# Kernel tuning notes

Hardware: AMD Instinct MI355X
Metric: run time of the kernel (lower is better)

## Reference

```python
import jax, jax.numpy as jnp
import numpy as np

N, C, T, V = 32, 128, 128, 25
HS, HT, CI = 3, 2, 32
BN_INV = float(1.0 / np.sqrt(1.0 + 1e-5))  # eval-mode BN: running_mean=0, running_var=1


def conv1x1(x, w, b):
    # x: (N,C,T,V), w: (O,C), b: (O,)
    return jnp.einsum('nctv,oc->notv', x, w) + b[None, :, None, None]


def bn(x, g, b):
    return x * (g * BN_INV)[None, :, None, None] + b[None, :, None, None]


def lrelu(x):
    return jax.nn.leaky_relu(x, 0.1)


def setup_inputs() -> dict:
    key = jax.random.key(0)
    ks = jax.random.split(key, 16)
    w = lambda k, shp: jax.random.normal(k, shp, dtype=jnp.float32) * 0.05
    inp = {
        'x': jax.random.normal(ks[0], (N, C, T, V), dtype=jnp.float32),
        # spatial attention QK projection (conv 1x1): 2*HS*CI out channels
        'w_in_s': w(ks[1], (2 * HS * CI, C)), 'b_in_s': jnp.zeros((2 * HS * CI,), jnp.float32),
        'attention0s': jnp.ones((1, HS, V, V), jnp.float32) / V,
        'alphas': jnp.ones((1, HS, 1, 1), jnp.float32),
        'w_out_s': w(ks[2], (C, HS * C)), 'b_out_s': jnp.zeros((C,), jnp.float32),
        'g_out_s': jnp.ones((C,), jnp.float32), 'be_out_s': jnp.zeros((C,), jnp.float32),
        'w_ff_s': w(ks[3], (C, C)), 'b_ff_s': jnp.zeros((C,), jnp.float32),
        'g_ff_s': jnp.ones((C,), jnp.float32), 'be_ff_s': jnp.zeros((C,), jnp.float32),
        # temporal attention QK projection: 4*HT*CI out channels
        'w_in_t': w(ks[4], (4 * HT * CI, C)), 'b_in_t': jnp.zeros((4 * HT * CI,), jnp.float32),
        'alphat_f': jnp.ones((1, HT, 1, 1), jnp.float32),
        'alphat_b': jnp.ones((1, HT, 1, 1), jnp.float32),
        'w_out_t': w(ks[5], (C, 2 * HT * C)), 'b_out_t': jnp.zeros((C,), jnp.float32),
        'g_out_t': jnp.ones((C,), jnp.float32), 'be_out_t': jnp.zeros((C,), jnp.float32),
        'w_ff_t': w(ks[6], (C, C)), 'b_ff_t': jnp.zeros((C,), jnp.float32),
        'g_ff_t': jnp.ones((C,), jnp.float32), 'be_ff_t': jnp.zeros((C,), jnp.float32),
        # TCN: 7x1 temporal conv
        'w_tcn': w(ks[7], (C, C, 7, 1)), 'b_tcn': jnp.zeros((C,), jnp.float32),
        'g_tcn': jnp.ones((C,), jnp.float32), 'be_tcn': jnp.zeros((C,), jnp.float32),
    }
    return inp


def reference(x, w_in_s, b_in_s, attention0s, alphas, w_out_s, b_out_s, g_out_s, be_out_s,
              w_ff_s, b_ff_s, g_ff_s, be_ff_s, w_in_t, b_in_t, alphat_f, alphat_b,
              w_out_t, b_out_t, g_out_t, be_out_t, w_ff_t, b_ff_t, g_ff_t, be_ff_t,
              w_tcn, b_tcn, g_tcn, be_tcn):
    n = x.shape[0]
    # ---------------- spatial attention (S_atten='free', glo_reg_s) ----------------
    att_bias = attention0s[:, :, None]            # (1,HS,1,V,V) broadcast over T
    alphas_u = alphas[:, :, None]                 # (1,HS,1,1,1)
    qk = conv1x1(x, w_in_s, b_in_s).reshape(n, 2 * HS, CI, T, V)
    q, k = qk[:, :HS], qk[:, HS:]
    att = att_bias + jnp.tanh(jnp.einsum('nsctu,nsctv->nstuv', q, k) / CI) * alphas_u  # (N,HS,T,V,V)
    y = jnp.einsum('nctu,nstuv->nsctv', x, att).reshape(n, HS * C, T, V)
    y = bn(conv1x1(y, w_out_s, b_out_s), g_out_s, be_out_s)
    y = lrelu(x + y)                               # downs1 = identity (in==out, stride 1)
    y = bn(conv1x1(y, w_ff_s, b_ff_s), g_ff_s, be_ff_s)
    s_out = lrelu(x + y)                           # downs2 = identity
    # ---------------- temporal attention (directed, T_atten='context') ----------------
    z_in = s_out                                   # parallel=False -> temporal eats s_out
    qk_t = conv1x1(z_in, w_in_t, b_in_t).reshape(n, 4 * HT, CI, T, V)
    qt, kt = qk_t[:, :2 * HT], qk_t[:, 2 * HT:]
    qt = qt.mean(-1)                               # context attention: mean over joints -> (N,2HT,CI,T)
    kt = kt.mean(-1)
    att_t = jnp.tanh(jnp.einsum('nsct,nscu->nstu', qt, kt) / CI)  # (N,2HT,T,T)
    backward_mask = jnp.triu(jnp.ones((T, T), jnp.float32))
    forward_mask = backward_mask.T
    att_f = att_t[:, :HT] * alphat_f * forward_mask
    att_b = att_t[:, HT:] * alphat_b * backward_mask
    att_t = jnp.concatenate([att_f, att_b], axis=1)               # (N,2HT,T,T)
    z = jnp.einsum('nctv,nstu->nscuv', z_in, att_t).reshape(n, 2 * HT * C, T, V)
    z = bn(conv1x1(z, w_out_t, b_out_t), g_out_t, be_out_t)
    z = lrelu(z_in + z)                            # downt1 = identity
    z = bn(conv1x1(z, w_ff_t, b_ff_t), g_ff_t, be_ff_t)
    t_out = lrelu(z_in + z)                        # downt2 = identity
    # ---------------- TCN branch ----------------
    z2 = jax.lax.conv_general_dilated(t_out, w_tcn, (1, 1), ((3, 3), (0, 0)),
                                      dimension_numbers=('NCHW', 'OIHW', 'NCHW'))
    z2 = bn(z2 + b_tcn[None, :, None, None] * 0 + b_tcn[None, :, None, None], g_tcn, be_tcn) if False else bn(z2 + b_tcn[None, :, None, None], g_tcn, be_tcn)
    out = lrelu(t_out + z2)                        # downtTCN = identity
    return out
```

## Files before the change

### kernel.cpp

```cpp
#include <hip/hip_runtime.h>
#include <cstddef>

#define Nn 32
#define Cc 128
#define Tt 128
#define Vv 25
#define BN_INV 0.9999950000374997f


typedef __attribute__((ext_vector_type(8))) short bf16x8;
typedef __attribute__((ext_vector_type(4))) float f32x4;

__device__ __forceinline__ unsigned short f2bf(float f) {
    union { float f; unsigned u; } x; x.f = f;
    return (unsigned short)((x.u + 0x7FFFu + ((x.u >> 16) & 1u)) >> 16);
}
__device__ __forceinline__ float bf2f(unsigned short s) {
    union { unsigned u; float f; } x; x.u = ((unsigned)s) << 16;
    return x.f;
}

template<int BMODE, int DMODE, int OM>
__global__ __launch_bounds__(256, 2) void gemm_k(
    const unsigned short* __restrict__ A, const void* __restrict__ Bv,
    float* __restrict__ D, unsigned short* __restrict__ Dbf,
    const float* __restrict__ resp, const float* __restrict__ bias,
    const float* __restrict__ gg, const float* __restrict__ bb,
    int M, int K, int lda, int ldb, int ldd,
    long an_stride, long bn_stride, long dn_stride, int gn)
{
    __shared__ short Al[8*64*8];
    __shared__ short Bl[8*64*8];

    const int n  = blockIdx.y;
    const int mt = blockIdx.x / gn;
    const int nt = blockIdx.x - mt*gn;
    const int m0 = mt*128;
    const int j0 = nt*128;

    const unsigned short* An = A + (size_t)n*an_stride;

    const int tid = threadIdx.x;
    const int wav = tid >> 6, lane = tid & 63;
    const int lq = lane >> 4, l16 = lane & 15;

    const int sm  = tid >> 1, skh = tid & 1;
    const int scol = tid & 127, skq = tid >> 7;
    const int bcol = j0 + scol;

    int bo = 0, bv_ = 0;
    if (BMODE == 3) { bo = bcol/25; bv_ = bcol - 25*bo; }

    f32x4 acc[2][8];
    #pragma unroll
    for (int i = 0; i < 2; ++i)
        #pragma unroll
        for (int c = 0; c < 8; ++c) acc[i][c] = (f32x4){0.f,0.f,0.f,0.f};

    for (int k0 = 0; k0 < K; k0 += 32) {
        bf16x8 a0 = (bf16x8){0,0,0,0,0,0,0,0}, a1 = a0;
        {
            int mg = m0 + sm;
            if (mg < M) {
                const unsigned short* ap = An + (size_t)mg*lda + k0 + skh*16;
                a0 = *(const bf16x8*)ap;
                a1 = *(const bf16x8*)(ap + 8);
            }
        }
        unsigned short bq[16];
        if (BMODE == 0) {
            const unsigned short* Bn = (const unsigned short*)Bv + (size_t)n*bn_stride;
            #pragma unroll
            for (int j = 0; j < 16; ++j)
                bq[j] = Bn[(size_t)(k0 + skq*16 + j)*ldb + bcol];
        } else if (BMODE == 4) {
            const float* Bf = (const float*)Bv + (size_t)n*bn_stride;
            #pragma unroll
            for (int j = 0; j < 16; ++j)
                bq[j] = f2bf(Bf[(size_t)(k0 + skq*16 + j)*ldb + bcol]);
        } else if (BMODE == 1) {
            const unsigned short* Bn = (const unsigned short*)Bv + (size_t)n*bn_stride;
            int kb = k0 + skq*16;
            int kidx = kb >> 7, c0 = kb & 127;
            int e = bcol + (kidx - 3)*25;
            bool ok = ((unsigned)e < 3200u);
            #pragma unroll
            for (int j = 0; j < 16; ++j)
                bq[j] = ok ? Bn[(size_t)(c0 + j)*3200 + e] : (unsigned short)0;
        } else {
            const unsigned short* Bn = (const unsigned short*)Bv + (size_t)n*bn_stride;
            int kb = k0 + skq*16;
            int h = kb >> 7, t0 = kb & 127;
            const unsigned short* bp = Bn + (size_t)h*409600 + (size_t)bo*3200
                                          + (size_t)t0*25 + bv_;
            #pragma unroll
            for (int j = 0; j < 16; ++j) bq[j] = bp[j*25];
        }

        __syncthreads();
        {
            short* Ap = Al + ((size_t)((sm>>4)*64 + (sm&15) + 32*skh))*8;
            *(bf16x8*)Ap = a0;
            *(bf16x8*)(Ap + 128) = a1;
        }
        {
            short* Bp = Bl + ((size_t)((scol>>4)*64 + (scol&15) + 32*skq))*8;
            bf16x8 p0, p1;
            #pragma unroll
            for (int j = 0; j < 8; ++j) { p0[j] = (short)bq[j]; p1[j] = (short)bq[8+j]; }
            *(bf16x8*)Bp = p0;
            *(bf16x8*)(Bp + 128) = p1;
        }
        __syncthreads();

        bf16x8 afr[2], bfr[8];
        afr[0] = *(const bf16x8*)(Al + ((size_t)((2*wav+0)*64 + lane))*8);
        afr[1] = *(const bf16x8*)(Al + ((size_t)((2*wav+1)*64 + lane))*8);
        #pragma unroll
        for (int c = 0; c < 8; ++c)
            bfr[c] = *(const bf16x8*)(Bl + ((size_t)(c*64 + lane))*8);
        #pragma unroll
        for (int i = 0; i < 2; ++i)
            #pragma unroll
            for (int c = 0; c < 8; ++c)
                acc[i][c] = __builtin_amdgcn_mfma_f32_16x16x32_bf16(
                    afr[i], bfr[c], acc[i][c], 0, 0, 0);
    }

    #pragma unroll
    for (int i = 0; i < 2; ++i) {
        const int mbase = m0 + (2*wav + i)*16 + lq*4;
        #pragma unroll
        for (int ct = 0; ct < 8; ++ct) {
            const int col = j0 + ct*16 + l16;
            if (DMODE == 0) {
                #pragma unroll
                for (int r = 0; r < 4; ++r) {
                    const int mg = mbase + r;
                    if (mg < M) {
                        const size_t addr = (size_t)mg*ldd + col + (size_t)n*dn_stride;
                        float val = acc[i][ct][r] + (bias ? bias[mg] : 0.f);
                        if (gg) {
                            val = val*(gg[mg]*BN_INV) + bb[mg] + resp[addr];
                            val = val > 0.f ? val : 0.1f*val;
                        }
                        if (OM != 1) D[addr] = val;
                        if (OM >= 1) Dbf[addr] = f2bf(val);
                    }
                }
            } else {
                const int c = col/25, v = col - 25*c;
                const float bi = bias ? bias[c] : 0.f;
                float gv = 0.f, b2 = 0.f;
                if (gg) { gv = gg[c]*BN_INV; b2 = bb[c]; }
                #pragma unroll
                for (int r = 0; r < 4; ++r) {
                    const int u = mbase + r;
                    const size_t addr = (size_t)c*3200 + (size_t)u*25 + v
                                      + (size_t)n*dn_stride;
                    float val = acc[i][ct][r] + bi;
                    if (gg) {
                        val = val*gv + b2 + resp[addr];
                        val = val > 0.f ? val : 0.1f*val;
                    }
                    if (OM != 1) D[addr] = val;
                    if (OM >= 1) Dbf[addr] = f2bf(val);
                }
            }
        }
    }
}

__global__ void k_prep(const float* __restrict__ wis, const float* __restrict__ wos,
                       const float* __restrict__ wfs, const float* __restrict__ wit,
                       const float* __restrict__ wot, const float* __restrict__ wft,
                       const float* __restrict__ wtc, unsigned short* __restrict__ W) {
    int i = blockIdx.x*256 + threadIdx.x;
    if (i < 24576) { W[i] = f2bf(wis[i]); return; }          i -= 24576;
    if (i < 49152) { W[24576 + i] = f2bf(wos[i]); return; }  i -= 49152;
    if (i < 16384) { W[73728 + i] = f2bf(wfs[i]); return; }  i -= 16384;
    if (i < 32768) { W[90112 + i] = f2bf(wit[i]); return; }  i -= 32768;
    if (i < 65536) {
        int ho = i >> 7, c = i & 127; int h = ho >> 7, o = ho & 127;
        W[122880 + i] = f2bf(wot[o*512 + h*128 + c]); return; } i -= 65536;
    if (i < 16384) { W[188416 + i] = f2bf(wft[i]); return; } i -= 16384;
    if (i < 114688) {
        int o = i / 896; int r = i - o*896; int kidx = r >> 7, c = r & 127;
        W[204800 + i] = f2bf(wtc[(o*128 + c)*7 + kidx]); }
}

__global__ void k_att_s(const unsigned short* __restrict__ qk,
                        const float* __restrict__ att0,
                        const float* __restrict__ alphas,
                        unsigned short* __restrict__ att) {
    int b = blockIdx.x;
    int n = b / (3*Tt); int rem = b - n*(3*Tt); int s = rem / Tt; int t = rem - s*Tt;
    __shared__ float qs[32*Vv], ks[32*Vv];
    const unsigned short* qp = qk + (size_t)n*614400 + (size_t)(s*32)*3200 + t*25;
    const unsigned short* kp = qk + (size_t)n*614400 + (size_t)(96 + s*32)*3200 + t*25;
    for (int i = threadIdx.x; i < 32*Vv; i += 256) {
        int c = i / Vv, v = i - c*Vv;
        qs[i] = bf2f(qp[(size_t)c*3200 + v]);
        ks[i] = bf2f(kp[(size_t)c*3200 + v]);
    }
    __syncthreads();
    float alpha = alphas[s];
    for (int i = threadIdx.x; i < Vv*Vv; i += 256) {
        int u = i / Vv, v = i - u*Vv;
        float a = 0.f;
        #pragma unroll
        for (int c = 0; c < 32; ++c) a += qs[c*Vv + u] * ks[c*Vv + v];
        att[(size_t)n*240000 + (size_t)s*80000 + (size_t)t*625 + i] =
            f2bf(att0[s*625 + i] + tanhf(a * (1.f/32.f)) * alpha);
    }
}

__global__ __launch_bounds__(256, 2) void k_eins_mfma(
    const float* __restrict__ X, const unsigned short* __restrict__ att,
    unsigned short* __restrict__ y2)
{
    __shared__ short Xf[128*128];
    __shared__ short Bf[7*4*64*8];

    const int n  = blockIdx.x >> 5;
    const int t0 = (blockIdx.x & 31) * 4;
    const int tid = threadIdx.x;
    const int wav = tid >> 6, lane = tid & 63;
    const int lq = lane >> 4, l16 = lane & 15;

    for (int i = tid; i < 7*4*64; i += 256)
        *(bf16x8*)(Bf + (size_t)i*8) = (bf16x8){0,0,0,0,0,0,0,0};

    const float* xp = X + (size_t)n*409600;
    for (int i = tid; i < 8192; i += 256) {
        int u2 = (i & 15)*2, tl = (i >> 4) & 3, c = i >> 6;
        float f0 = 0.f, f1 = 0.f;
        if (u2 < 25) {
            const float* p = xp + (size_t)c*3200 + (t0 + tl)*25 + u2;
            f0 = p[0];
            if (u2 < 24) f1 = p[1];
        }
        unsigned pk = (unsigned)f2bf(f0) | ((unsigned)f2bf(f1) << 16);
        int byte = (i*4) ^ ((c & 7) << 4);
        *(unsigned*)((char*)Xf + byte) = pk;
    }
    __syncthreads();

    bf16x8 afr[2][4];
    #pragma unroll
    for (int i = 0; i < 2; ++i) {
        const int c = (2*wav + i)*16 + l16;
        #pragma unroll
        for (int ks = 0; ks < 4; ++ks) {
            int byte = ((c*128 + ks*32 + lq*8)*2) ^ ((c & 7) << 4);
            afr[i][ks] = *(const bf16x8*)((const char*)Xf + byte);
        }
    }

    for (int s = 0; s < 3; ++s) {
        const unsigned short* ap = att + (size_t)n*240000 + (size_t)s*80000
                                       + (size_t)t0*625;
        for (int j = tid; j < 2500; j += 256) {
            int tl = j / 625, r = j - tl*625;
            int u = r / 25, v = r - u*25;
            int col = tl*25 + v;
            int l = ((u >> 3) << 4) | (col & 15);
            int nt = col >> 4;
            Bf[(size_t)((nt*4 + tl)*64 + l)*8 + (u & 7)] = (short)ap[j];
        }
        __syncthreads();

        f32x4 acc[2][7];
        #pragma unroll
        for (int i = 0; i < 2; ++i)
            #pragma unroll
            for (int nt = 0; nt < 7; ++nt) acc[i][nt] = (f32x4){0.f,0.f,0.f,0.f};

        #pragma unroll
        for (int ks = 0; ks < 4; ++ks) {
            bf16x8 bfr[7];
            #pragma unroll
            for (int nt = 0; nt < 7; ++nt)
                bfr[nt] = *(const bf16x8*)(Bf + (size_t)((nt*4 + ks)*64 + lane)*8);
            #pragma unroll
            for (int i = 0; i < 2; ++i)
                #pragma unroll
                for (int nt = 0; nt < 7; ++nt)
                    acc[i][nt] = __builtin_amdgcn_mfma_f32_16x16x32_bf16(
                        afr[i][ks], bfr[nt], acc[i][nt], 0, 0, 0);
        }

        unsigned short* yb = y2 + (size_t)n*1228800 + (size_t)(s*128)*3200 + t0*25;
        #pragma unroll
        for (int i = 0; i < 2; ++i) {
            const int row = (2*wav + i)*16 + lq*4;
            #pragma unroll
            for (int nt = 0; nt < 7; ++nt) {
                const int col = nt*16 + l16;
                if (col < 100) {
                    unsigned short* yp = yb + (size_t)row*3200 + col;
                    #pragma unroll
                    for (int r = 0; r < 4; ++r)
                        yp[(size_t)r*3200] = f2bf(acc[i][nt][r]);
                }
            }
        }
        __syncthreads();
    }
}

__global__ void k_mean(const float* __restrict__ X, unsigned short* __restrict__ xb) {
    int idx = blockIdx.x*256 + threadIdx.x;
    if (idx >= Nn*Cc*Tt) return;
    const float* p = X + (size_t)idx*25;
    float s = 0.f;
    #pragma unroll
    for (int v = 0; v < Vv; ++v) s += p[v];
    xb[idx] = f2bf(s * (1.f/25.f));
}

__global__ void k_att_t(const float* __restrict__ qkt, const float* __restrict__ af,
                        const float* __restrict__ ab, unsigned short* __restrict__ attb) {
    int n = blockIdx.x >> 2, h = blockIdx.x & 3;
    __shared__ float qs[32*Tt], ks[32*Tt];
    const float* qp = qkt + (size_t)n*32768 + (size_t)(h*32)*128;
    const float* kp = qkt + (size_t)n*32768 + (size_t)(128 + h*32)*128;
    for (int i = threadIdx.x; i < 32*Tt; i += 256) { qs[i] = qp[i]; ks[i] = kp[i]; }
    __syncthreads();
    float alpha = (h < 2) ? af[h] : ab[h-2];
    for (int i = threadIdx.x; i < Tt*Tt; i += 256) {
        int u = i >> 7, t = i & 127;
        bool keep = (h < 2) ? (t >= u) : (t <= u);
        float val = 0.f;
        if (keep) {
            float a = 0.f;
            #pragma unroll
            for (int c = 0; c < 32; ++c) a += qs[c*Tt + t] * ks[c*Tt + u];
            val = tanhf(a * (1.f/32.f)) * alpha;
        }
        attb[(size_t)n*65536 + (size_t)u*512 + h*128 + t] = f2bf(val);
    }
}

extern "C" void kernel_launch(void* const* d_in, const int* in_sizes, int n_in,
                              void* d_out, int out_size, void* d_ws, size_t ws_size,
                              hipStream_t stream) {
    const float* x       = (const float*)d_in[0];
    const float* w_in_s  = (const float*)d_in[1];
    const float* b_in_s  = (const float*)d_in[2];
    const float* att0s   = (const float*)d_in[3];
    const float* alphas  = (const float*)d_in[4];
    const float* w_out_s = (const float*)d_in[5];
    const float* b_out_s = (const float*)d_in[6];
    const float* g_out_s = (const float*)d_in[7];
    const float* be_out_s= (const float*)d_in[8];
    const float* w_ff_s  = (const float*)d_in[9];
    const float* b_ff_s  = (const float*)d_in[10];
    const float* g_ff_s  = (const float*)d_in[11];
    const float* be_ff_s = (const float*)d_in[12];
    const float* w_in_t  = (const float*)d_in[13];
    const float* b_in_t  = (const float*)d_in[14];
    const float* alphat_f= (const float*)d_in[15];
    const float* alphat_b= (const float*)d_in[16];
    const float* w_out_t = (const float*)d_in[17];
    const float* b_out_t = (const float*)d_in[18];
    const float* g_out_t = (const float*)d_in[19];
    const float* be_out_t= (const float*)d_in[20];
    const float* w_ff_t  = (const float*)d_in[21];
    const float* b_ff_t  = (const float*)d_in[22];
    const float* g_ff_t  = (const float*)d_in[23];
    const float* be_ff_t = (const float*)d_in[24];
    const float* w_tcn   = (const float*)d_in[25];
    const float* b_tcn   = (const float*)d_in[26];
    const float* g_tcn   = (const float*)d_in[27];
    const float* be_tcn  = (const float*)d_in[28];

    hipMemsetAsync(d_ws, 0, ws_size, stream);

    float* ws = (float*)d_ws;
    unsigned short* WB    = (unsigned short*)ws;
    unsigned short* QKBF  = (unsigned short*)(ws + 200000);
    unsigned short* S1BF  = (unsigned short*)(ws + 200000);
    unsigned short* ATSB  = (unsigned short*)(ws + 10030400);
    unsigned short* Y2BF  = (unsigned short*)(ws + 13870400);
    float*          SOUT  = ws + 33531200;
    unsigned short* ATTB  = (unsigned short*)(ws + 200000);
    unsigned short* XBARB = (unsigned short*)(ws + 1300000);
    float*          QKT   = ws + 1600000;
    unsigned short* TMPB  = (unsigned short*)(ws + 2700000);
    unsigned short* T1BF  = (unsigned short*)(ws + 46638400);
    float*          TOUT  = ws + 2700000;
    unsigned short* TOUTB = (unsigned short*)(ws + 15810000);
    float* out = (float*)d_out;

    unsigned short* wbis = WB;
    unsigned short* wbos = WB + 24576;
    unsigned short* wbfs = WB + 73728;
    unsigned short* wbit = WB + 90112;
    unsigned short* wbot = WB + 122880;
    unsigned short* wbft = WB + 188416;
    unsigned short* wbtc = WB + 204800;

    dim3 blk(256);
    const float* NUL = nullptr;

    k_prep<<<1248, blk, 0, stream>>>(w_in_s, w_out_s, w_ff_s, w_in_t,
                                     w_out_t, w_ff_t, w_tcn, WB);

    gemm_k<4,0,1><<<dim3(50,32), blk, 0, stream>>>(
        wbis, x, nullptr, QKBF, NUL, b_in_s, NUL, NUL,
        192, 128, 128, 3200, 3200, 0L, 409600L, 614400L, 25);
    k_att_s<<<Nn*3*Tt, blk, 0, stream>>>(QKBF, att0s, alphas, ATSB);
    k_eins_mfma<<<dim3(Nn*32), blk, 0, stream>>>(x, ATSB, Y2BF);
    gemm_k<0,0,1><<<dim3(25,32), blk, 0, stream>>>(
        wbos, Y2BF, nullptr, S1BF, x, b_out_s, g_out_s, be_out_s,
        128, 384, 384, 3200, 3200, 0L, 1228800L, 409600L, 25);
    gemm_k<0,0,0><<<dim3(25,32), blk, 0, stream>>>(
        wbfs, S1BF, SOUT, nullptr, x, b_ff_s, g_ff_s, be_ff_s,
        128, 128, 128, 3200, 3200, 0L, 409600L, 409600L, 25);

    k_mean<<<2048, blk, 0, stream>>>(SOUT, XBARB);
    gemm_k<0,0,0><<<dim3(2,32), blk, 0, stream>>>(
        wbit, XBARB, QKT, nullptr, NUL, b_in_t, NUL, NUL,
        256, 128, 128, 128, 128, 0L, 16384L, 32768L, 1);
    k_att_t<<<Nn*4, blk, 0, stream>>>(QKT, alphat_f, alphat_b, ATTB);
    gemm_k<4,0,1><<<dim3(100,32), blk, 0, stream>>>(
        wbot, SOUT, nullptr, TMPB, NUL, NUL, NUL, NUL,
        512, 128, 128, 3200, 3200, 0L, 409600L, 1638400L, 25);
    gemm_k<3,2,1><<<dim3(25,32), blk, 0, stream>>>(
        ATTB, TMPB, nullptr, T1BF, SOUT, b_out_t, g_out_t, be_out_t,
        128, 512, 512, 3200, 3200, 65536L, 1638400L, 409600L, 25);
    gemm_k<0,0,2><<<dim3(25,32), blk, 0, stream>>>(
        wbft, T1BF, TOUT, TOUTB, SOUT, b_ff_t, g_ff_t, be_ff_t,
        128, 128, 128, 3200, 3200, 0L, 409600L, 409600L, 25);

    gemm_k<1,0,0><<<dim3(25,32), blk, 0, stream>>>(
        wbtc, TOUTB, out, nullptr, TOUT, b_tcn, g_tcn, be_tcn,
        128, 896, 896, 3200, 3200, 0L, 409600L, 409600L, 25);
}
```

Measured before the change: 762.7 us.

## Halve GEMM N-tile to 64 and prefetch next K-slice into registers

The shared GEMM kernel now uses a 128x64 output tile instead of 128x128, which doubles the grid size for every GEMM launch and raises launch bounds to four blocks per SM. It also adds register double-buffering: the next K-slice's A and B values are loaded from global memory after the LDS barrier, so those loads overlap the MFMA work on the current slice. The aim is more occupancy and latency hiding for these memory-bound 1x1-conv GEMMs. The cost is lower data reuse per tile (A is re-read twice as often) and more register pressure under the tighter launch bound.

```diff
diff --git a/kernel.cpp b/kernel.cpp
--- a/kernel.cpp
+++ b/kernel.cpp
@@ -20,8 +20,50 @@
     return x.f;
 }
 
+
+#define GFETCH(K0)                                                             \
+    {                                                                          \
+        int mg = m0 + sm;                                                      \
+        if (mg < M) {                                                          \
+            const unsigned short* ap = An + (size_t)mg*lda + (K0) + skh*16;    \
+            a0n = *(const bf16x8*)ap;                                          \
+            a1n = *(const bf16x8*)(ap + 8);                                    \
+        }                                                                      \
+        if (BMODE == 0) {                                                      \
+            const unsigned short* Bn = (const unsigned short*)Bv               \
+                                     + (size_t)n*bn_stride;                    \
+            _Pragma("unroll")                                                  \
+            for (int j = 0; j < 8; ++j)                                        \
+                bqn[j] = Bn[(size_t)((K0) + skq*8 + j)*ldb + bcol];            \
+        } else if (BMODE == 4) {                                               \
+            const float* Bf = (const float*)Bv + (size_t)n*bn_stride;          \
+            _Pragma("unroll")                                                  \
+            for (int j = 0; j < 8; ++j)                                        \
+                bqn[j] = f2bf(Bf[(size_t)((K0) + skq*8 + j)*ldb + bcol]);      \
+        } else if (BMODE == 1) {                                               \
+            const unsigned short* Bn = (const unsigned short*)Bv               \
+                                     + (size_t)n*bn_stride;                    \
+            int kb = (K0) + skq*8;                                             \
+            int kidx = kb >> 7, c0 = kb & 127;                                 \
+            int e = bcol + (kidx - 3)*25;                                      \
+            bool ok = ((unsigned)e < 3200u);                                   \
+            _Pragma("unroll")                                                  \
+            for (int j = 0; j < 8; ++j)                                        \
+                bqn[j] = ok ? Bn[(size_t)(c0 + j)*3200 + e] : (unsigned short)0;\
+        } else {                                                  \
+            const unsigned short* Bn = (const unsigned short*)Bv               \
+                                     + (size_t)n*bn_stride;                    \
+            int kb = (K0) + skq*8;                                             \
+            int h = kb >> 7, t0b = kb & 127;                                   \
+            const unsigned short* bp = Bn + (size_t)h*409600 + (size_t)bo*3200 \
+                                          + (size_t)t0b*25 + bv_;              \
+            _Pragma("unroll")                                                  \
+            for (int j = 0; j < 8; ++j) bqn[j] = bp[j*25];                     \
+        }                                                                      \
+    }
+
 template<int BMODE, int DMODE, int OM>
-__global__ __launch_bounds__(256, 2) void gemm_k(
+__global__ __launch_bounds__(256, 4) void gemm_k(
     const unsigned short* __restrict__ A, const void* __restrict__ Bv,
     float* __restrict__ D, unsigned short* __restrict__ Dbf,
     const float* __restrict__ resp, const float* __restrict__ bias,
@@ -30,13 +72,13 @@
     long an_stride, long bn_stride, long dn_stride, int gn)
 {
     __shared__ short Al[8*64*8];
-    __shared__ short Bl[8*64*8];
+    __shared__ short Bl[4*64*8];
 
     const int n  = blockIdx.y;
     const int mt = blockIdx.x / gn;
     const int nt = blockIdx.x - mt*gn;
     const int m0 = mt*128;
-    const int j0 = nt*128;
+    const int j0 = nt*64;
 
     const unsigned short* An = A + (size_t)n*an_stride;
 
@@ -45,84 +87,50 @@
     const int lq = lane >> 4, l16 = lane & 15;
 
     const int sm  = tid >> 1, skh = tid & 1;
-    const int scol = tid & 127, skq = tid >> 7;
+    const int scol = tid & 63, skq = tid >> 6;
     const int bcol = j0 + scol;
 
     int bo = 0, bv_ = 0;
     if (BMODE == 3) { bo = bcol/25; bv_ = bcol - 25*bo; }
 
-    f32x4 acc[2][8];
+    f32x4 acc[2][4];
     #pragma unroll
     for (int i = 0; i < 2; ++i)
         #pragma unroll
-        for (int c = 0; c < 8; ++c) acc[i][c] = (f32x4){0.f,0.f,0.f,0.f};
+        for (int c = 0; c < 4; ++c) acc[i][c] = (f32x4){0.f,0.f,0.f,0.f};
+
+    bf16x8 a0n = (bf16x8){0,0,0,0,0,0,0,0}, a1n = a0n;
+    unsigned short bqn[8];
+    GFETCH(0);
 
     for (int k0 = 0; k0 < K; k0 += 32) {
-        bf16x8 a0 = (bf16x8){0,0,0,0,0,0,0,0}, a1 = a0;
-        {
-            int mg = m0 + sm;
-            if (mg < M) {
-                const unsigned short* ap = An + (size_t)mg*lda + k0 + skh*16;
-                a0 = *(const bf16x8*)ap;
-                a1 = *(const bf16x8*)(ap + 8);
-            }
-        }
-        unsigned short bq[16];
-        if (BMODE == 0) {
-            const unsigned short* Bn = (const unsigned short*)Bv + (size_t)n*bn_stride;
-            #pragma unroll
-            for (int j = 0; j < 16; ++j)
-                bq[j] = Bn[(size_t)(k0 + skq*16 + j)*ldb + bcol];
-        } else if (BMODE == 4) {
-            const float* Bf = (const float*)Bv + (size_t)n*bn_stride;
-            #pragma unroll
-            for (int j = 0; j < 16; ++j)
-                bq[j] = f2bf(Bf[(size_t)(k0 + skq*16 + j)*ldb + bcol]);
-        } else if (BMODE == 1) {
-            const unsigned short* Bn = (const unsigned short*)Bv + (size_t)n*bn_stride;
-            int kb = k0 + skq*16;
-            int kidx = kb >> 7, c0 = kb & 127;
-            int e = bcol + (kidx - 3)*25;
-            bool ok = ((unsigned)e < 3200u);
-            #pragma unroll
-            for (int j = 0; j < 16; ++j)
-                bq[j] = ok ? Bn[(size_t)(c0 + j)*3200 + e] : (unsigned short)0;
-        } else {
-            const unsigned short* Bn = (const unsigned short*)Bv + (size_t)n*bn_stride;
-            int kb = k0 + skq*16;
-            int h = kb >> 7, t0 = kb & 127;
-            const unsigned short* bp = Bn + (size_t)h*409600 + (size_t)bo*3200
-                                          + (size_t)t0*25 + bv_;
-            #pragma unroll
-            for (int j = 0; j < 16; ++j) bq[j] = bp[j*25];
-        }
-
         __syncthreads();
         {
             short* Ap = Al + ((size_t)((sm>>4)*64 + (sm&15) + 32*skh))*8;
-            *(bf16x8*)Ap = a0;
-            *(bf16x8*)(Ap + 128) = a1;
+            *(bf16x8*)Ap = a0n;
+            *(bf16x8*)(Ap + 128) = a1n;
         }
         {
-            short* Bp = Bl + ((size_t)((scol>>4)*64 + (scol&15) + 32*skq))*8;
-            bf16x8 p0, p1;
-            #pragma unroll
-            for (int j = 0; j < 8; ++j) { p0[j] = (short)bq[j]; p1[j] = (short)bq[8+j]; }
+            short* Bp = Bl + ((size_t)((scol>>4)*64 + skq*16 + (scol&15)))*8;
+            bf16x8 p0;
+            #pragma unroll
+            for (int j = 0; j < 8; ++j) p0[j] = (short)bqn[j];
             *(bf16x8*)Bp = p0;
-            *(bf16x8*)(Bp + 128) = p1;
         }
         __syncthreads();
 
-        bf16x8 afr[2], bfr[8];
+        if (k0 + 32 < K) GFETCH(k0 + 32);
+
+        bf16x8 afr[2], bfr[4];
         afr[0] = *(const bf16x8*)(Al + ((size_t)((2*wav+0)*64 + lane))*8);
         afr[1] = *(const bf16x8*)(Al + ((size_t)((2*wav+1)*64 + lane))*8);
         #pragma unroll
-        for (int c = 0; c < 8; ++c)
+        for (int c = 0; c < 4; ++c)
             bfr[c] = *(const bf16x8*)(Bl + ((size_t)(c*64 + lane))*8);
         #pragma unroll
         for (int i = 0; i < 2; ++i)
             #pragma unroll
-            for (int c = 0; c < 8; ++c)
+            for (int c = 0; c < 4; ++c)
                 acc[i][c] = __builtin_amdgcn_mfma_f32_16x16x32_bf16(
                     afr[i], bfr[c], acc[i][c], 0, 0, 0);
     }
@@ -131,7 +139,7 @@
     for (int i = 0; i < 2; ++i) {
         const int mbase = m0 + (2*wav + i)*16 + lq*4;
         #pragma unroll
-        for (int ct = 0; ct < 8; ++ct) {
+        for (int ct = 0; ct < 4; ++ct) {
             const int col = j0 + ct*16 + l16;
             if (DMODE == 0) {
                 #pragma unroll
@@ -407,34 +415,34 @@
     k_prep<<<1248, blk, 0, stream>>>(w_in_s, w_out_s, w_ff_s, w_in_t,
                                      w_out_t, w_ff_t, w_tcn, WB);
 
-    gemm_k<4,0,1><<<dim3(50,32), blk, 0, stream>>>(
+    gemm_k<4,0,1><<<dim3(100,32), blk, 0, stream>>>(
         wbis, x, nullptr, QKBF, NUL, b_in_s, NUL, NUL,
-        192, 128, 128, 3200, 3200, 0L, 409600L, 614400L, 25);
+        192, 128, 128, 3200, 3200, 0L, 409600L, 614400L, 50);
     k_att_s<<<Nn*3*Tt, blk, 0, stream>>>(QKBF, att0s, alphas, ATSB);
     k_eins_mfma<<<dim3(Nn*32), blk, 0, stream>>>(x, ATSB, Y2BF);
-    gemm_k<0,0,1><<<dim3(25,32), blk, 0, stream>>>(
+    gemm_k<0,0,1><<<dim3(50,32), blk, 0, stream>>>(
         wbos, Y2BF, nullptr, S1BF, x, b_out_s, g_out_s, be_out_s,
-        128, 384, 384, 3200, 3200, 0L, 1228800L, 409600L, 25);
-    gemm_k<0,0,0><<<dim3(25,32), blk, 0, stream>>>(
+        128, 384, 384, 3200, 3200, 0L, 1228800L, 409600L, 50);
+    gemm_k<0,0,0><<<dim3(50,32), blk, 0, stream>>>(
         wbfs, S1BF, SOUT, nullptr, x, b_ff_s, g_ff_s, be_ff_s,
-        128, 128, 128, 3200, 3200, 0L, 409600L, 409600L, 25);
+        128, 128, 128, 3200, 3200, 0L, 409600L, 409600L, 50);
 
     k_mean<<<2048, blk, 0, stream>>>(SOUT, XBARB);
-    gemm_k<0,0,0><<<dim3(2,32), blk, 0, stream>>>(
+    gemm_k<0,0,0><<<dim3(4,32), blk, 0, stream>>>(
         wbit, XBARB, QKT, nullptr, NUL, b_in_t, NUL, NUL,
-        256, 128, 128, 128, 128, 0L, 16384L, 32768L, 1);
+        256, 128, 128, 128, 128, 0L, 16384L, 32768L, 2);
     k_att_t<<<Nn*4, blk, 0, stream>>>(QKT, alphat_f, alphat_b, ATTB);
-    gemm_k<4,0,1><<<dim3(100,32), blk, 0, stream>>>(
+    gemm_k<4,0,1><<<dim3(200,32), blk, 0, stream>>>(
         wbot, SOUT, nullptr, TMPB, NUL, NUL, NUL, NUL,
-        512, 128, 128, 3200, 3200, 0L, 409600L, 1638400L, 25);
-    gemm_k<3,2,1><<<dim3(25,32), blk, 0, stream>>>(
+        512, 128, 128, 3200, 3200, 0L, 409600L, 1638400L, 50);
+    gemm_k<3,2,1><<<dim3(50,32), blk, 0, stream>>>(
         ATTB, TMPB, nullptr, T1BF, SOUT, b_out_t, g_out_t, be_out_t,
-        128, 512, 512, 3200, 3200, 65536L, 1638400L, 409600L, 25);
-    gemm_k<0,0,2><<<dim3(25,32), blk, 0, stream>>>(
+        128, 512, 512, 3200, 3200, 65536L, 1638400L, 409600L, 50);
+    gemm_k<0,0,2><<<dim3(50,32), blk, 0, stream>>>(
         wbft, T1BF, TOUT, TOUTB, SOUT, b_ff_t, g_ff_t, be_ff_t,
-        128, 128, 128, 3200, 3200, 0L, 409600L, 409600L, 25);
-
-    gemm_k<1,0,0><<<dim3(25,32), blk, 0, stream>>>(
+        128, 128, 128, 3200, 3200, 0L, 409600L, 409600L, 50);
+
+    gemm_k<1,0,0><<<dim3(50,32), blk, 0, stream>>>(
         wbtc, TOUTB, out, nullptr, TOUT, b_tcn, g_tcn, be_tcn,
-        128, 896, 896, 3200, 3200, 0L, 409600L, 409600L, 25);
-}
+        128, 896, 896, 3200, 3200, 0L, 409600L, 409600L, 50);
+}
```

New measurement: 767.7 us. About the same (+0.7%).
